# Kernel tuning notes

Measured on AMD Instinct MI355X. Metric: run time of the kernel, lower is better.

## Reference

```python
import jax, jax.numpy as jnp
import numpy as np

EPS = 1e-6
B, T, C = 2, 1024, 2048
H, KV, D = 32, 8, 128
E, F, TOPK = 8, 768, 2


def rmsnorm(x, w):
    xf = x.astype(jnp.float32)
    var = jnp.mean(xf * xf, axis=-1, keepdims=True)
    return w * (xf * jax.lax.rsqrt(var + EPS)).astype(x.dtype)


def rotate_half(x):
    d = x.shape[-1] // 2
    return jnp.concatenate([-x[..., d:], x[..., :d]], axis=-1)


def setup_inputs() -> dict:
    key = jax.random.key(0)
    ks = jax.random.split(key, 12)
    sc = 0.02
    x = jax.random.normal(ks[0], (B, T, C), dtype=jnp.float32)
    # RoPE tables: cos/sin of shape [B, T, D]
    inv_freq = 1.0 / (1e6 ** (np.arange(0, D, 2, dtype=np.float32) / D))
    pos = np.arange(T, dtype=np.float32)
    freqs = pos[:, None] * inv_freq[None, :]          # [T, D/2]
    emb = np.concatenate([freqs, freqs], axis=-1)     # [T, D]
    cos = jnp.broadcast_to(jnp.cos(emb)[None], (B, T, D)).astype(jnp.float32)
    sin = jnp.broadcast_to(jnp.sin(emb)[None], (B, T, D)).astype(jnp.float32)
    return {
        "x": x, "cos": cos, "sin": sin,
        "ln1_w": jnp.ones((C,), jnp.float32),
        "q_w": jax.random.normal(ks[1], (C, H * D), jnp.float32) * sc,
        "k_w": jax.random.normal(ks[2], (C, KV * D), jnp.float32) * sc,
        "v_w": jax.random.normal(ks[3], (C, KV * D), jnp.float32) * sc,
        "o_w": jax.random.normal(ks[4], (H * D, C), jnp.float32) * sc,
        "qn_w": jnp.ones((D,), jnp.float32),
        "kn_w": jnp.ones((D,), jnp.float32),
        "ln2_w": jnp.ones((C,), jnp.float32),
        "gate_w": jax.random.normal(ks[5], (C, E), jnp.float32) * sc,
        "gate_up_w": jax.random.normal(ks[6], (E, C, 2 * F), jnp.float32) * sc,
        "down_w": jax.random.normal(ks[7], (E, F, C), jnp.float32) * sc,
    }


def reference(x, cos, sin, ln1_w, q_w, k_w, v_w, o_w, qn_w, kn_w, ln2_w,
              gate_w, gate_up_w, down_w):
    b, t, c = x.shape
    # ---- attention branch ----
    h = rmsnorm(x, ln1_w)
    q = (h @ q_w).reshape(b, t, H, D)
    k = (h @ k_w).reshape(b, t, KV, D)
    v = (h @ v_w).reshape(b, t, KV, D)
    q = rmsnorm(q, qn_w)
    k = rmsnorm(k, kn_w)
    cb = cos[:, :, None, :]
    sb = sin[:, :, None, :]
    q = q * cb + rotate_half(q) * sb
    k = k * cb + rotate_half(k) * sb
    rep = H // KV
    k = jnp.repeat(k, rep, axis=2)  # [b,t,H,D]
    v = jnp.repeat(v, rep, axis=2)
    scores = jnp.einsum('bthd,bshd->bhts', q, k) / jnp.sqrt(jnp.float32(D))
    causal = jnp.tril(jnp.ones((t, t), dtype=bool))
    scores = jnp.where(causal, scores, jnp.finfo(scores.dtype).min)
    attn = jax.nn.softmax(scores, axis=-1)
    ao = jnp.einsum('bhts,bshd->bthd', attn, v).reshape(b, t, H * D) @ o_w
    x = x + ao
    # ---- MoE branch ----
    h2 = rmsnorm(x, ln2_w)
    hidden = h2.reshape(-1, c)                     # [N, C]
    logits = hidden @ gate_w                       # [N, E]
    rw = jax.nn.softmax(logits.astype(jnp.float32), axis=-1)
    tw, ti = jax.lax.top_k(rw, TOPK)
    tw = tw / (tw.sum(axis=-1, keepdims=True) + 1e-9)
    n = hidden.shape[0]
    routed = jnp.zeros_like(logits).at[jnp.arange(n)[:, None], ti].set(tw.astype(logits.dtype))
    routed = routed / (routed.sum(axis=-1, keepdims=True) + 1e-9)
    gu = jnp.einsum('th,ehq->teq', hidden, gate_up_w)   # [N, E, 2F]
    g, u = jnp.split(gu, 2, axis=-1)
    eo = jnp.einsum('teq,eqh->teh', jax.nn.silu(g) * u, down_w)  # [N, E, C]
    moe = (eo * routed[..., None]).sum(axis=1).reshape(b, t, c)
    return x + moe
```

## Files before the change

kernel.cpp:

```cpp
#include <hip/hip_runtime.h>
#include <hip/hip_bf16.h>

typedef short bf16x8 __attribute__((ext_vector_type(8)));
typedef float f32x4 __attribute__((ext_vector_type(4)));
typedef unsigned short u16;

#define NTOK 2048
#define CDIM 2048
#define TSEQ 1024
#define NH   32
#define NKV  8
#define DH   128
#define NE   8
#define FDIM 768
#define CAP  2048

#define GLOAD_LDS16(g, l) \
  __builtin_amdgcn_global_load_lds((const __attribute__((address_space(1))) void*)(g), \
                                   (__attribute__((address_space(3))) void*)(l), 16, 0, 0)

__device__ __forceinline__ u16 f2bf(float f){
  union { float f; unsigned u; } v; v.f = f;
  unsigned r = v.u + 0x7FFFu + ((v.u >> 16) & 1u);
  return (u16)(r >> 16);
}
__device__ __forceinline__ float bf2f(u16 x){
  union { unsigned u; float f; } v; v.u = ((unsigned)x) << 16; return v.f;
}

__device__ __forceinline__ f32x4 mfma_bf16(bf16x8 a, bf16x8 b, f32x4 c){
  return __builtin_amdgcn_mfma_f32_16x16x32_bf16(a, b, c, 0, 0, 0);
}

__device__ __forceinline__ int xcd_swz(int orig, int nwg){
  int xcd = orig & 7;
  int q = nwg >> 3, r = nwg & 7;
  int base = (xcd < r) ? xcd*(q+1) : r*(q+1) + (xcd-r)*q;
  return base + (orig >> 3);
}

__global__ void cast_transpose(const float* __restrict__ in, u16* __restrict__ out,
                               int R, int Cc, int rstride, int d1,
                               long long s_hi, long long s_lo)
{
  __shared__ u16 tile[64][72];
  int z = blockIdx.z;
  in  += (long long)(z / d1) * s_hi + (long long)(z % d1) * s_lo;
  out += (size_t)z * R * Cc;
  int r0 = blockIdx.y*64, c0 = blockIdx.x*64;
  int lr = threadIdx.x >> 4;
  int lc = (threadIdx.x & 15) * 4;
  #pragma unroll
  for(int i=0;i<4;i++){
    int r = lr + i*16;
    float4 v = *(const float4*)(in + (size_t)(r0 + r)*rstride + c0 + lc);
    tile[lc+0][r] = f2bf(v.x);
    tile[lc+1][r] = f2bf(v.y);
    tile[lc+2][r] = f2bf(v.z);
    tile[lc+3][r] = f2bf(v.w);
  }
  __syncthreads();
  int oc  = threadIdx.x >> 2;
  int orr = (threadIdx.x & 3) * 16;
  uint4 a  = *(const uint4*)&tile[oc][orr];
  uint4 b2 = *(const uint4*)&tile[oc][orr + 8];
  *(uint4*)(out + (size_t)(c0+oc)*R + r0 + orr)     = a;
  *(uint4*)(out + (size_t)(c0+oc)*R + r0 + orr + 8) = b2;
}

__global__ void cast_transpose_qkv(const float* __restrict__ qw, const float* __restrict__ kw,
                                   const float* __restrict__ vw, u16* __restrict__ wqkvT)
{
  __shared__ u16 tile[64][72];
  int bx = blockIdx.x;
  const float* in; u16* out; int rstride, c0;
  if(bx < 64){       in = qw; out = wqkvT;                        rstride = 4096; c0 = bx*64; }
  else if(bx < 80){  in = kw; out = wqkvT + (size_t)4096*2048;    rstride = 1024; c0 = (bx-64)*64; }
  else {             in = vw; out = wqkvT + (size_t)5120*2048;    rstride = 1024; c0 = (bx-80)*64; }
  const int R = 2048;
  int r0 = blockIdx.y*64;
  int lr = threadIdx.x >> 4;
  int lc = (threadIdx.x & 15) * 4;
  #pragma unroll
  for(int i=0;i<4;i++){
    int r = lr + i*16;
    float4 v = *(const float4*)(in + (size_t)(r0 + r)*rstride + c0 + lc);
    tile[lc+0][r] = f2bf(v.x);
    tile[lc+1][r] = f2bf(v.y);
    tile[lc+2][r] = f2bf(v.z);
    tile[lc+3][r] = f2bf(v.w);
  }
  __syncthreads();
  int oc  = threadIdx.x >> 2;
  int orr = (threadIdx.x & 3) * 16;
  uint4 a  = *(const uint4*)&tile[oc][orr];
  uint4 b2 = *(const uint4*)&tile[oc][orr + 8];
  *(uint4*)(out + (size_t)(c0+oc)*R + r0 + orr)     = a;
  *(uint4*)(out + (size_t)(c0+oc)*R + r0 + orr + 8) = b2;
}

__global__ void transpose_gate(const float* __restrict__ gw, float* __restrict__ gwT)
{
  int i = blockIdx.x*256 + threadIdx.x;
  int c = i >> 3, e = i & 7;
  gwT[(size_t)e*CDIM + c] = gw[(size_t)c*NE + e];
}

__global__ void transpose_u16(const u16* __restrict__ in, u16* __restrict__ out,
                              int R, int Cc, int rstride, int d1,
                              long long s_hi, long long s_lo)
{
  __shared__ u16 tile[32][34];
  int z = blockIdx.z;
  in += (long long)(z / d1) * s_hi + (long long)(z % d1) * s_lo;
  out += (size_t)z * R * Cc;
  int tx = threadIdx.x & 31, ty = threadIdx.x >> 5;
  int r0 = blockIdx.y * 32, c0 = blockIdx.x * 32;
  #pragma unroll
  for(int i=0;i<4;i++){
    int r = r0 + ty + i*8;
    if(r < R && c0 + tx < Cc) tile[ty + i*8][tx] = in[(size_t)r * rstride + c0 + tx];
  }
  __syncthreads();
  #pragma unroll
  for(int i=0;i<4;i++){
    int c = c0 + ty + i*8;
    if(c < Cc && r0 + tx < R) out[(size_t)c * R + r0 + tx] = tile[tx][ty + i*8];
  }
}

__global__ void rmsnorm_kernel(const float* __restrict__ x, const float* __restrict__ w,
                               u16* __restrict__ outb, float* __restrict__ outf)
{
  __shared__ float sbuf[4];
  int row = blockIdx.x;
  const float* xr = x + (size_t)row * CDIM;
  int t0 = threadIdx.x * 8;
  float4 v0 = *(const float4*)(xr + t0);
  float4 v1 = *(const float4*)(xr + t0 + 4);
  float a[8] = {v0.x,v0.y,v0.z,v0.w,v1.x,v1.y,v1.z,v1.w};
  float ss = 0.f;
  #pragma unroll
  for(int i=0;i<8;i++) ss += a[i]*a[i];
  #pragma unroll
  for(int o=32;o>0;o>>=1) ss += __shfl_xor(ss, o);
  if((threadIdx.x & 63) == 0) sbuf[threadIdx.x >> 6] = ss;
  __syncthreads();
  float tot = sbuf[0]+sbuf[1]+sbuf[2]+sbuf[3];
  float r = rsqrtf(tot * (1.0f/CDIM) + 1e-6f);
  float4 w0 = *(const float4*)(w + t0);
  float4 w1 = *(const float4*)(w + t0 + 4);
  float wv[8] = {w0.x,w0.y,w0.z,w0.w,w1.x,w1.y,w1.z,w1.w};
  #pragma unroll
  for(int i=0;i<8;i++){
    float o = a[i] * r * wv[i];
    outb[(size_t)row*CDIM + t0 + i] = f2bf(o);
    if(outf) outf[(size_t)row*CDIM + t0 + i] = o;
  }
}

__global__ __launch_bounds__(512, 1) void gemm256(const u16* __restrict__ A,
                                                  const u16* __restrict__ Bt,
                                                  u16* __restrict__ Cb,
                                                  int M, int N, int K)
{
  extern __shared__ u16 lds[];
  const int NT = K >> 6;
  int tid = threadIdx.x;
  int lane = tid & 63, g = lane >> 4, cl = lane & 15;
  int wid = tid >> 6, wr = wid >> 2, wc = wid & 3;
  int br = blockIdx.y * 256, bc = blockIdx.x * 192;
  int rowl[4], slotl[4], srcoff[4];
  #pragma unroll
  for(int l=0;l<4;l++){
    int c = l*512 + tid;
    rowl[l]  = c >> 3;
    slotl[l] = c & 7;
    srcoff[l] = (slotl[l] ^ (rowl[l] & 7)) * 8;
  }
  f32x4 acc[8][3];
  #pragma unroll
  for(int m=0;m<8;m++)
    #pragma unroll
    for(int n=0;n<3;n++) acc[m][n] = (f32x4){0.f,0.f,0.f,0.f};

  auto stage = [&](int t, int b){
    int k0 = t << 6;
    #pragma unroll
    for(int l=0;l<4;l++)
      GLOAD_LDS16(A  + (size_t)(br + rowl[l])*K + k0 + srcoff[l],
                  &lds[b*16384 + rowl[l]*64 + slotl[l]*8]);
    #pragma unroll
    for(int l=0;l<3;l++)
      GLOAD_LDS16(Bt + (size_t)(bc + rowl[l])*K + k0 + srcoff[l],
                  &lds[32768 + b*12288 + rowl[l]*64 + slotl[l]*8]);
  };

  stage(0, 0);
  for(int t=0;t<NT;t++){
    int buf = t & 1;
    if(t+1 < NT){
      stage(t+1, buf^1);
      asm volatile("s_waitcnt vmcnt(7)" ::: "memory");
    } else {
      asm volatile("s_waitcnt vmcnt(0)" ::: "memory");
    }
    asm volatile("s_barrier" ::: "memory");
    const u16* As_ = &lds[buf*16384];
    const u16* Bs_ = &lds[32768 + buf*12288];
    __builtin_amdgcn_s_setprio(1);
    #pragma unroll
    for(int kk=0;kk<2;kk++){
      bf16x8 a[8], b[3];
      #pragma unroll
      for(int m=0;m<8;m++){
        int row = wr*128 + m*16 + cl;
        int sl  = ((4*kk + g) ^ (row & 7)) * 8;
        a[m] = *(const bf16x8*)&As_[row*64 + sl];
      }
      #pragma unroll
      for(int n=0;n<3;n++){
        int row = wc*48 + n*16 + cl;
        int sl  = ((4*kk + g) ^ (row & 7)) * 8;
        b[n] = *(const bf16x8*)&Bs_[row*64 + sl];
      }
      #pragma unroll
      for(int m=0;m<8;m++)
        #pragma unroll
        for(int n=0;n<3;n++)
          acc[m][n] = mfma_bf16(a[m], b[n], acc[m][n]);
    }
    __builtin_amdgcn_s_setprio(0);
    asm volatile("s_barrier" ::: "memory");
  }
  #pragma unroll
  for(int m=0;m<8;m++)
    #pragma unroll
    for(int n=0;n<3;n++)
      #pragma unroll
      for(int j=0;j<4;j++){
        int row = br + wr*128 + m*16 + g*4 + j;
        int col = bc + wc*48 + n*16 + cl;
        Cb[(size_t)row*N + col] = f2bf(acc[m][n][j]);
      }
}

__global__ __launch_bounds__(256) void gemm_oproj_pipe(const u16* __restrict__ A,
                                                       const u16* __restrict__ Bt,
                                                       float* __restrict__ C,
                                                       const float* __restrict__ addsrc,
                                                       int M, int N, int K)
{
  extern __shared__ u16 lds[];
  int nwg = gridDim.x;
  int wgid = xcd_swz(blockIdx.x, nwg);
  int nbx = N >> 7;
  int bys = wgid / nbx, bxs = wgid % nbx;
  const int NT = K >> 6;
  int tid = threadIdx.x;
  int lane = tid&63, g = lane>>4, cl = lane&15;
  int w = tid>>6, wr = w>>1, wc = w&1;
  int br = bys*128, bc = bxs*128;
  int rowc[4], slotc[4], srcoff[4];
  #pragma unroll
  for(int l=0;l<4;l++){
    int c = l*256 + tid;
    rowc[l]  = c >> 3;
    slotc[l] = c & 7;
    srcoff[l] = (slotc[l] ^ (rowc[l] & 7)) * 8;
  }
  f32x4 acc[4][4];
  #pragma unroll
  for(int m=0;m<4;m++)
    #pragma unroll
    for(int n=0;n<4;n++) acc[m][n] = (f32x4){0.f,0.f,0.f,0.f};

  auto stage = [&](int t, int b){
    int k0 = t << 6;
    #pragma unroll
    for(int l=0;l<4;l++)
      GLOAD_LDS16(A + (size_t)(br + rowc[l])*K + k0 + srcoff[l],
                  &lds[b*8192 + rowc[l]*64 + slotc[l]*8]);
    #pragma unroll
    for(int l=0;l<4;l++)
      GLOAD_LDS16(Bt + (size_t)(bc + rowc[l])*K + k0 + srcoff[l],
                  &lds[16384 + b*8192 + rowc[l]*64 + slotc[l]*8]);
  };

  stage(0, 0);
  for(int t=0;t<NT;t++){
    int buf = t & 1;
    if(t+1 < NT){
      stage(t+1, buf^1);
      asm volatile("s_waitcnt vmcnt(8)" ::: "memory");
    } else {
      asm volatile("s_waitcnt vmcnt(0)" ::: "memory");
    }
    asm volatile("s_barrier" ::: "memory");
    const u16* As_ = &lds[buf*8192];
    const u16* Bs_ = &lds[16384 + buf*8192];
    __builtin_amdgcn_s_setprio(1);
    #pragma unroll
    for(int kk=0;kk<2;kk++){
      bf16x8 a[4], b[4];
      #pragma unroll
      for(int m=0;m<4;m++){
        int row = wr*64 + m*16 + cl;
        int sl  = ((4*kk + g) ^ (row & 7)) * 8;
        a[m] = *(const bf16x8*)&As_[row*64 + sl];
      }
      #pragma unroll
      for(int n=0;n<4;n++){
        int row = wc*64 + n*16 + cl;
        int sl  = ((4*kk + g) ^ (row & 7)) * 8;
        b[n] = *(const bf16x8*)&Bs_[row*64 + sl];
      }
      #pragma unroll
      for(int m=0;m<4;m++)
        #pragma unroll
        for(int n=0;n<4;n++)
          acc[m][n] = mfma_bf16(a[m], b[n], acc[m][n]);
    }
    __builtin_amdgcn_s_setprio(0);
    asm volatile("s_barrier" ::: "memory");
  }
  #pragma unroll
  for(int m=0;m<4;m++)
    #pragma unroll
    for(int n=0;n<4;n++)
      #pragma unroll
      for(int j=0;j<4;j++){
        int row = br + wr*64 + m*16 + g*4 + j;
        int col = bc + wc*64 + n*16 + cl;
        C[(size_t)row*N + col] = acc[m][n][j] + addsrc[(size_t)row*N + col];
      }
}

__global__ void qk_norm_rope(const u16* __restrict__ qkv, const float* __restrict__ cosb,
                             const float* __restrict__ sinb, const float* __restrict__ qnw,
                             const float* __restrict__ knw,
                             u16* __restrict__ qb, u16* __restrict__ kb)
{
  __shared__ float red[2];
  __shared__ float buf[128];
  int bt = blockIdx.x;
  int head = blockIdx.y;
  int d = threadIdx.x;
  int b = bt >> 10, t = bt & 1023;
  bool isq = head < NH;
  const u16* src = qkv + (size_t)bt*6144 + (isq ? head*DH : 4096 + (head-NH)*DH);
  float v = bf2f(src[d]);
  float ss = v*v;
  #pragma unroll
  for(int o=32;o>0;o>>=1) ss += __shfl_xor(ss, o);
  if((threadIdx.x & 63) == 0) red[threadIdx.x >> 6] = ss;
  __syncthreads();
  float tot = red[0] + red[1];
  float r = rsqrtf(tot * (1.0f/DH) + 1e-6f);
  float nv = v * r * (isq ? qnw[d] : knw[d]);
  buf[d] = nv;
  __syncthreads();
  float rot = (d < 64) ? -buf[d+64] : buf[d-64];
  float cs = cosb[(size_t)bt*DH + d], sn = sinb[(size_t)bt*DH + d];
  float ov = nv*cs + rot*sn;
  if(isq) ov *= 0.08838834764831845f;
  if(isq) qb[(((size_t)b*NH  + head)     *TSEQ + t)*DH + d] = f2bf(ov);
  else    kb[(((size_t)b*NKV + (head-NH))*TSEQ + t)*DH + d] = f2bf(ov);
}

__global__ __launch_bounds__(256) void attn_kernel(const u16* __restrict__ qb,
                                                   const u16* __restrict__ kb,
                                                   const u16* __restrict__ vt,
                                                   u16* __restrict__ aob)
{
  __shared__ u16 Ks[64*128];
  __shared__ u16 Vs[144*64];
  __shared__ u16 Ps[4][32][72];
  int tid = threadIdx.x;
  int w = tid>>6, lane = tid&63, g = lane>>4, cl = lane&15;
  int nwg = gridDim.x * gridDim.y * gridDim.z;
  int orig = (blockIdx.z * gridDim.y + blockIdx.y) * gridDim.x + blockIdx.x;
  int wgid = xcd_swz(orig, nwg);
  int bxs = wgid % gridDim.x;
  int bys = (wgid / gridDim.x) % gridDim.y;
  int bzs = wgid / (gridDim.x * gridDim.y);
  int b = bzs, kvh = bys;
  int qt = (gridDim.x - 1) - bxs;
  int q0 = qt*32;
  int h = kvh*4 + w;
  const u16* qp = qb + (((size_t)b*NH  + h  )*TSEQ)*DH;
  const u16* kp = kb + (((size_t)b*NKV + kvh)*TSEQ)*DH;
  const u16* vp = vt + (((size_t)b*NKV + kvh)*DH)*TSEQ;
  for(int idx = tid; idx < 16*64; idx += 256){
    int r = idx >> 6, c2 = idx & 63;
    Vs[(128 + r)*64 + c2] = (r == 0) ? (u16)0x3F80 : (u16)0;
  }
  int kRow[4], kDst[4], kSrc[4], vRow[4], vDst[4], vSrc[4];
  #pragma unroll
  for(int it=0; it<4; it++){
    int c = tid + it*256;
    kRow[it] = c >> 4;
    int ks = c & 15;
    kDst[it] = kRow[it]*128 + ks*8;
    kSrc[it] = (ks ^ (kRow[it] & 7)) * 8;
    vRow[it] = c >> 3;
    int vs = c & 7;
    vDst[it] = vRow[it]*64 + vs*8;
    vSrc[it] = (vs ^ (vRow[it] & 7)) * 8;
  }
  bf16x8 aq[2][4];
  #pragma unroll
  for(int m=0;m<2;m++)
    #pragma unroll
    for(int kd=0;kd<4;kd++)
      aq[m][kd] = *(const bf16x8*)(qp + (size_t)(q0 + m*16 + cl)*DH + kd*32 + g*8);
  f32x4 accO[2][9];
  #pragma unroll
  for(int m=0;m<2;m++)
    #pragma unroll
    for(int n=0;n<9;n++) accO[m][n] = (f32x4){0.f,0.f,0.f,0.f};
  float mr[2][4];
  #pragma unroll
  for(int m=0;m<2;m++)
    #pragma unroll
    for(int j=0;j<4;j++) mr[m][j] = -1e30f;
  for(int kv0 = 0; kv0 < q0 + 32; kv0 += 64){
    #pragma unroll
    for(int it=0; it<4; it++){
      GLOAD_LDS16(kp + (size_t)(kv0 + kRow[it])*DH + kSrc[it], &Ks[kDst[it]]);
      GLOAD_LDS16(vp + (size_t)vRow[it]*TSEQ + kv0 + vSrc[it], &Vs[vDst[it]]);
    }
    __syncthreads();
    f32x4 sc[2][4];
    #pragma unroll
    for(int m=0;m<2;m++)
      #pragma unroll
      for(int n=0;n<4;n++) sc[m][n] = (f32x4){0.f,0.f,0.f,0.f};
    __builtin_amdgcn_s_setprio(1);
    #pragma unroll
    for(int kd=0;kd<4;kd++){
      bf16x8 bk[4];
      #pragma unroll
      for(int n=0;n<4;n++){
        int row = n*16 + cl;
        bk[n] = *(const bf16x8*)&Ks[row*128 + (((kd*4 + g) ^ (cl & 7))*8)];
      }
      #pragma unroll
      for(int m=0;m<2;m++)
        #pragma unroll
        for(int n=0;n<4;n++)
          sc[m][n] = mfma_bf16(aq[m][kd], bk[n], sc[m][n]);
    }
    __builtin_amdgcn_s_setprio(0);
    if(kv0 + 63 > q0){
      #pragma unroll
      for(int m=0;m<2;m++)
        #pragma unroll
        for(int n=0;n<4;n++)
          #pragma unroll
          for(int j=0;j<4;j++){
            int row = q0 + m*16 + g*4 + j;
            int col = kv0 + n*16 + cl;
            if(col > row) sc[m][n][j] = -1e30f;
          }
    }
    float tmax[2][4];
    #pragma unroll
    for(int m=0;m<2;m++)
      #pragma unroll
      for(int j=0;j<4;j++)
        tmax[m][j] = fmaxf(fmaxf(sc[m][0][j], sc[m][1][j]), fmaxf(sc[m][2][j], sc[m][3][j]));
    #pragma unroll
    for(int o=1;o<16;o<<=1)
      #pragma unroll
      for(int m=0;m<2;m++)
        #pragma unroll
        for(int j=0;j<4;j++) tmax[m][j] = fmaxf(tmax[m][j], __shfl_xor(tmax[m][j], o));
    float grow = -1e30f;
    #pragma unroll
    for(int m=0;m<2;m++)
      #pragma unroll
      for(int j=0;j<4;j++) grow = fmaxf(grow, tmax[m][j] - mr[m][j]);
    grow = fmaxf(grow, __shfl_xor(grow, 16));
    grow = fmaxf(grow, __shfl_xor(grow, 32));
    if(grow > 8.0f){
      #pragma unroll
      for(int m=0;m<2;m++)
        #pragma unroll
        for(int j=0;j<4;j++){
          float mn = fmaxf(mr[m][j], tmax[m][j]);
          float f  = __expf(mr[m][j] - mn);
          mr[m][j] = mn;
          #pragma unroll
          for(int n=0;n<9;n++) accO[m][n][j] *= f;
        }
    }
    #pragma unroll
    for(int m=0;m<2;m++)
      #pragma unroll
      for(int n=0;n<4;n++)
        #pragma unroll
        for(int j=0;j<4;j++)
          sc[m][n][j] = __expf(sc[m][n][j] - mr[m][j]);
    #pragma unroll
    for(int m=0;m<2;m++)
      #pragma unroll
      for(int n=0;n<4;n++)
        #pragma unroll
        for(int j=0;j<4;j++)
          Ps[w][m*16 + g*4 + j][n*16 + cl] = f2bf(sc[m][n][j]);
    bf16x8 pa[2][2];
    #pragma unroll
    for(int m=0;m<2;m++)
      #pragma unroll
      for(int s2=0;s2<2;s2++)
        pa[m][s2] = *(const bf16x8*)&Ps[w][m*16 + cl][s2*32 + g*8];
    __builtin_amdgcn_s_setprio(1);
    #pragma unroll
    for(int n=0;n<9;n++){
      #pragma unroll
      for(int s2=0;s2<2;s2++){
        bf16x8 bv = *(const bf16x8*)&Vs[(n*16 + cl)*64 + (((s2*4 + g) ^ (cl & 7))*8)];
        #pragma unroll
        for(int m=0;m<2;m++)
          accO[m][n] = mfma_bf16(pa[m][s2], bv, accO[m][n]);
      }
    }
    __builtin_amdgcn_s_setprio(0);
    __syncthreads();
  }
  #pragma unroll
  for(int m=0;m<2;m++){
    float linv[4];
    #pragma unroll
    for(int j=0;j<4;j++){
      float l = __shfl(accO[m][8][j], lane & 48);
      linv[j] = 1.0f / l;
    }
    #pragma unroll
    for(int n=0;n<8;n++)
      #pragma unroll
      for(int j=0;j<4;j++){
        int row = q0 + m*16 + g*4 + j;
        float v = accO[m][n][j] * linv[j];
        aob[((size_t)b*TSEQ + row)*(NH*DH) + h*DH + n*16 + cl] = f2bf(v);
      }
  }
}

__global__ void route_kernel(const float* __restrict__ h2f, const float* __restrict__ gwT,
                             int* __restrict__ cnt, int* __restrict__ bidx,
                             float* __restrict__ bw)
{
  int lane = threadIdx.x & 63;
  int token = blockIdx.x*4 + (threadIdx.x >> 6);
  float acc[8];
  #pragma unroll
  for(int e=0;e<8;e++) acc[e]=0.f;
  for(int c0 = lane*4; c0 < CDIM; c0 += 256){
    float4 hv = *(const float4*)(h2f + (size_t)token*CDIM + c0);
    #pragma unroll
    for(int e=0;e<8;e++){
      float4 gv = *(const float4*)(gwT + (size_t)e*CDIM + c0);
      acc[e] += hv.x*gv.x + hv.y*gv.y + hv.z*gv.z + hv.w*gv.w;
    }
  }
  #pragma unroll
  for(int o=32;o>0;o>>=1)
    #pragma unroll
    for(int e=0;e<8;e++) acc[e] += __shfl_xor(acc[e], o);
  if(lane==0){
    float mx = acc[0];
    #pragma unroll
    for(int e=1;e<8;e++) mx = fmaxf(mx, acc[e]);
    float rw[8]; float s=0.f;
    #pragma unroll
    for(int e=0;e<8;e++){ rw[e] = __expf(acc[e]-mx); s += rw[e]; }
    #pragma unroll
    for(int e=0;e<8;e++) rw[e] /= s;
    int i0=0;
    #pragma unroll
    for(int e=1;e<8;e++) if(rw[e] > rw[i0]) i0=e;
    int i1 = (i0==0)?1:0;
    #pragma unroll
    for(int e=0;e<8;e++) if(e!=i0 && rw[e] > rw[i1]) i1=e;
    float tw0=rw[i0], tw1=rw[i1];
    float s1 = tw0+tw1+1e-9f;
    float a0 = tw0/s1, a1 = tw1/s1;
    float s2 = a0+a1+1e-9f;
    float w0 = a0/s2, w1 = a1/s2;
    int sl0 = atomicAdd(&cnt[i0],1);
    bidx[i0*CAP + sl0] = token; bw[i0*CAP + sl0] = w0;
    int sl1 = atomicAdd(&cnt[i1],1);
    bidx[i1*CAP + sl1] = token; bw[i1*CAP + sl1] = w1;
  }
}

__global__ __launch_bounds__(256) void gemm_gateup_pipe(const u16* __restrict__ h2b,
                                                        const u16* __restrict__ gupT,
                                                        u16* __restrict__ act,
                                                        const int* __restrict__ bidx,
                                                        const int* __restrict__ cnt)
{
  extern __shared__ u16 lds[];
  int d = blockIdx.x;
  int e = d & 7, j = d >> 3;
  int y = j / 12, x = j % 12;
  int nc = cnt[e];
  int sr = y*128;
  if(sr >= nc) return;
  const int K = CDIM, NT = K >> 6;
  const u16* Btg = gupT + (size_t)e*1536*CDIM + (size_t)(x*64)*CDIM;
  const u16* Btu = Btg + (size_t)768*CDIM;
  const int* be = bidx + e*CAP;
  int tid = threadIdx.x;
  int lane = tid&63, g = lane>>4, cl = lane&15;
  int w = tid>>6, wr = w>>1, wc = w&1;
  int rowA[4], slotA[4], srcA[4];
  long long atok[4];
  #pragma unroll
  for(int l=0;l<4;l++){
    int c = l*256 + tid;
    rowA[l]  = c >> 3;
    slotA[l] = c & 7;
    srcA[l] = (slotA[l] ^ (rowA[l] & 7)) * 8;
    int t = be[sr + rowA[l]];
    if(t < 0 || t >= NTOK) t = 0;
    atok[l] = (long long)t * CDIM;
  }
  int rowB[2], slotB[2], srcB[2];
  #pragma unroll
  for(int l=0;l<2;l++){
    int c = l*256 + tid;
    rowB[l]  = c >> 3;
    slotB[l] = c & 7;
    srcB[l] = (slotB[l] ^ (rowB[l] & 7)) * 8;
  }
  f32x4 accG[4][2], accU[4][2];
  #pragma unroll
  for(int m=0;m<4;m++)
    #pragma unroll
    for(int n=0;n<2;n++){ accG[m][n] = (f32x4){0.f,0.f,0.f,0.f}; accU[m][n] = (f32x4){0.f,0.f,0.f,0.f}; }

  auto stage = [&](int t, int b){
    int k0 = t << 6;
    #pragma unroll
    for(int l=0;l<4;l++)
      GLOAD_LDS16(h2b + atok[l] + k0 + srcA[l],
                  &lds[b*8192 + rowA[l]*64 + slotA[l]*8]);
    #pragma unroll
    for(int l=0;l<2;l++)
      GLOAD_LDS16(Btg + (size_t)rowB[l]*K + k0 + srcB[l],
                  &lds[16384 + b*4096 + rowB[l]*64 + slotB[l]*8]);
    #pragma unroll
    for(int l=0;l<2;l++)
      GLOAD_LDS16(Btu + (size_t)rowB[l]*K + k0 + srcB[l],
                  &lds[24576 + b*4096 + rowB[l]*64 + slotB[l]*8]);
  };

  stage(0, 0);
  for(int t=0;t<NT;t++){
    int buf = t & 1;
    if(t+1 < NT){
      stage(t+1, buf^1);
      asm volatile("s_waitcnt vmcnt(8)" ::: "memory");
    } else {
      asm volatile("s_waitcnt vmcnt(0)" ::: "memory");
    }
    asm volatile("s_barrier" ::: "memory");
    const u16* As_ = &lds[buf*8192];
    const u16* Bg_ = &lds[16384 + buf*4096];
    const u16* Bu_ = &lds[24576 + buf*4096];
    __builtin_amdgcn_s_setprio(1);
    #pragma unroll
    for(int kk=0;kk<2;kk++){
      bf16x8 a[4], bg[2], bu[2];
      #pragma unroll
      for(int m=0;m<4;m++){
        int row = wr*64 + m*16 + cl;
        int sl  = ((4*kk + g) ^ (row & 7)) * 8;
        a[m] = *(const bf16x8*)&As_[row*64 + sl];
      }
      #pragma unroll
      for(int n=0;n<2;n++){
        int row = wc*32 + n*16 + cl;
        int sl  = ((4*kk + g) ^ (row & 7)) * 8;
        bg[n] = *(const bf16x8*)&Bg_[row*64 + sl];
        bu[n] = *(const bf16x8*)&Bu_[row*64 + sl];
      }
      #pragma unroll
      for(int m=0;m<4;m++)
        #pragma unroll
        for(int n=0;n<2;n++){
          accG[m][n] = mfma_bf16(a[m], bg[n], accG[m][n]);
          accU[m][n] = mfma_bf16(a[m], bu[n], accU[m][n]);
        }
    }
    __builtin_amdgcn_s_setprio(0);
    asm volatile("s_barrier" ::: "memory");
  }
  #pragma unroll
  for(int m=0;m<4;m++)
    #pragma unroll
    for(int n=0;n<2;n++)
      #pragma unroll
      for(int jj=0;jj<4;jj++){
        int slot = sr + wr*64 + m*16 + g*4 + jj;
        int col  = x*64 + wc*32 + n*16 + cl;
        float gv = accG[m][n][jj], uv = accU[m][n][jj];
        float av = gv / (1.f + __expf(-gv)) * uv;
        act[((size_t)e*CAP + slot)*FDIM + col] = f2bf(av);
      }
}

__global__ __launch_bounds__(256) void gemm_down_pipe(const u16* __restrict__ act,
                                                      const u16* __restrict__ downT,
                                                      float* __restrict__ out,
                                                      const int* __restrict__ bidx,
                                                      const float* __restrict__ bw,
                                                      const int* __restrict__ cnt)
{
  extern __shared__ u16 lds[];
  int d = blockIdx.x;
  int e = d & 7, j = d >> 3;
  int y = j >> 4, x = j & 15;
  int nc = cnt[e];
  int sr = y*128;
  if(sr >= nc) return;
  const int K = FDIM, NT = K >> 6;
  const u16* A  = act   + ((size_t)e*CAP + sr)*FDIM;
  const u16* Bt = downT + (size_t)e*CDIM*FDIM + (size_t)(x*128)*FDIM;
  const int* be = bidx + e*CAP;
  const float* bwe = bw + e*CAP;
  int tid = threadIdx.x;
  int lane = tid&63, g = lane>>4, cl = lane&15;
  int w = tid>>6, wr = w>>1, wc = w&1;
  int rowc[4], slotc[4], srcoff[4];
  #pragma unroll
  for(int l=0;l<4;l++){
    int c = l*256 + tid;
    rowc[l]  = c >> 3;
    slotc[l] = c & 7;
    srcoff[l] = (slotc[l] ^ (rowc[l] & 7)) * 8;
  }
  f32x4 acc[4][4];
  #pragma unroll
  for(int m=0;m<4;m++)
    #pragma unroll
    for(int n=0;n<4;n++) acc[m][n] = (f32x4){0.f,0.f,0.f,0.f};

  auto stage = [&](int t, int b){
    int k0 = t << 6;
    #pragma unroll
    for(int l=0;l<4;l++)
      GLOAD_LDS16(A + (size_t)rowc[l]*K + k0 + srcoff[l],
                  &lds[b*8192 + rowc[l]*64 + slotc[l]*8]);
    #pragma unroll
    for(int l=0;l<4;l++)
      GLOAD_LDS16(Bt + (size_t)rowc[l]*K + k0 + srcoff[l],
                  &lds[16384 + b*8192 + rowc[l]*64 + slotc[l]*8]);
  };

  stage(0, 0);
  for(int t=0;t<NT;t++){
    int buf = t & 1;
    if(t+1 < NT){
      stage(t+1, buf^1);
      asm volatile("s_waitcnt vmcnt(8)" ::: "memory");
    } else {
      asm volatile("s_waitcnt vmcnt(0)" ::: "memory");
    }
    asm volatile("s_barrier" ::: "memory");
    const u16* As_ = &lds[buf*8192];
    const u16* Bs_ = &lds[16384 + buf*8192];
    __builtin_amdgcn_s_setprio(1);
    #pragma unroll
    for(int kk=0;kk<2;kk++){
      bf16x8 a[4], b[4];
      #pragma unroll
      for(int m=0;m<4;m++){
        int row = wr*64 + m*16 + cl;
        int sl  = ((4*kk + g) ^ (row & 7)) * 8;
        a[m] = *(const bf16x8*)&As_[row*64 + sl];
      }
      #pragma unroll
      for(int n=0;n<4;n++){
        int row = wc*64 + n*16 + cl;
        int sl  = ((4*kk + g) ^ (row & 7)) * 8;
        b[n] = *(const bf16x8*)&Bs_[row*64 + sl];
      }
      #pragma unroll
      for(int m=0;m<4;m++)
        #pragma unroll
        for(int n=0;n<4;n++)
          acc[m][n] = mfma_bf16(a[m], b[n], acc[m][n]);
    }
    __builtin_amdgcn_s_setprio(0);
    asm volatile("s_barrier" ::: "memory");
  }
  #pragma unroll
  for(int m=0;m<4;m++)
    #pragma unroll
    for(int jj=0;jj<4;jj++){
      int slot = sr + wr*64 + m*16 + g*4 + jj;
      if(slot < nc){
        int tok = be[slot];
        float wgt = bwe[slot];
        #pragma unroll
        for(int n=0;n<4;n++){
          int col = x*128 + wc*64 + n*16 + cl;
          atomicAdd(out + (size_t)tok*CDIM + col, wgt * acc[m][n][jj]);
        }
      }
    }
}

extern "C" void kernel_launch(void* const* d_in, const int* in_sizes, int n_in,
                              void* d_out, int out_size, void* d_ws, size_t ws_size,
                              hipStream_t stream)
{
  const float* x     = (const float*)d_in[0];
  const float* cosb  = (const float*)d_in[1];
  const float* sinb  = (const float*)d_in[2];
  const float* ln1w  = (const float*)d_in[3];
  const float* qw    = (const float*)d_in[4];
  const float* kw    = (const float*)d_in[5];
  const float* vw    = (const float*)d_in[6];
  const float* ow    = (const float*)d_in[7];
  const float* qnw   = (const float*)d_in[8];
  const float* knw   = (const float*)d_in[9];
  const float* ln2w  = (const float*)d_in[10];
  const float* gatew = (const float*)d_in[11];
  const float* gupw  = (const float*)d_in[12];
  const float* downw = (const float*)d_in[13];
  float* out = (float*)d_out;

  char* ws = (char*)d_ws;
  size_t off = 0;
  auto alloc = [&](size_t bytes)->char*{
    char* p = ws + off;
    off = (off + bytes + 255) & ~(size_t)255;
    return p;
  };
  u16*   wqkvT = (u16*)  alloc((size_t)6144*2048*2);
  u16*   owT   = (u16*)  alloc((size_t)2048*4096*2);
  u16*   gupT  = (u16*)  alloc((size_t)8*1536*2048*2);
  u16*   downT = (u16*)  alloc((size_t)8*2048*768*2);
  u16*   h1b   = (u16*)  alloc((size_t)2048*2048*2);
  u16*   qkvb  = (u16*)  alloc((size_t)2048*6144*2);
  u16*   qb    = (u16*)  alloc((size_t)2*32*1024*128*2);
  u16*   kb    = (u16*)  alloc((size_t)2*8*1024*128*2);
  u16*   vt    = (u16*)  alloc((size_t)2*8*1024*128*2);
  u16*   aob   = (u16*)  alloc((size_t)2048*4096*2);
  float* h2f   = (float*)alloc((size_t)2048*2048*4);
  u16*   h2b   = (u16*)  alloc((size_t)2048*2048*2);
  u16*   actb  = (u16*)  alloc((size_t)8*2048*768*2);
  int*   bidx  = (int*)  alloc((size_t)8*2048*4);
  float* bwgt  = (float*)alloc((size_t)8*2048*4);
  float* gwT   = (float*)alloc((size_t)8*2048*4);
  int*   cnt   = (int*)  alloc(64);
  (void)ws_size; (void)in_sizes; (void)n_in; (void)out_size;

  hipMemsetAsync(cnt, 0, 8*sizeof(int), stream);

  cast_transpose_qkv<<<dim3(96,32), 256, 0, stream>>>(qw, kw, vw, wqkvT);
  cast_transpose<<<dim3(32,64,1), 256, 0, stream>>>(ow, owT,      4096, 2048, 2048, 1, 0, 0);
  cast_transpose<<<dim3(24,32,8), 256, 0, stream>>>(gupw, gupT,   2048, 1536, 1536, 8, 0, (long long)2048*1536);
  cast_transpose<<<dim3(32,12,8), 256, 0, stream>>>(downw, downT, 768,  2048, 2048, 8, 0, (long long)768*2048);
  transpose_gate<<<64, 256, 0, stream>>>(gatew, gwT);

  rmsnorm_kernel<<<2048, 256, 0, stream>>>(x, ln1w, h1b, nullptr);
  gemm256<<<dim3(32,8), 512, 114688, stream>>>(h1b, wqkvT, qkvb, 2048, 6144, 2048);
  qk_norm_rope<<<dim3(2048,40), 128, 0, stream>>>(qkvb, cosb, sinb, qnw, knw, qb, kb);
  transpose_u16<<<dim3(4,32,16), 256, 0, stream>>>(qkvb + 5120, vt, 1024, 128, 6144, 8,
                                                   (long long)1024*6144, 128);
  attn_kernel<<<dim3(32,8,2), 256, 0, stream>>>(qb, kb, vt, aob);
  gemm_oproj_pipe<<<256, 256, 65536, stream>>>(aob, owT, out, x, 2048, 2048, 4096);
  rmsnorm_kernel<<<2048, 256, 0, stream>>>(out, ln2w, h2b, h2f);
  route_kernel<<<512, 256, 0, stream>>>(h2f, gwT, cnt, bidx, bwgt);
  gemm_gateup_pipe<<<1536, 256, 65536, stream>>>(h2b, gupT, actb, bidx, cnt);
  gemm_down_pipe<<<2048, 256, 65536, stream>>>(actb, downT, out, bidx, bwgt, cnt);
}
```

Baseline: 442.3 us.

## Replace 256x192 QKV GEMM with 128x128 tiles and XCD-swizzled 1D grid

The QKV projection GEMM moves from a 256x192 tile run by 512 threads (256 workgroups, one per CU) to a 128x128 tile run by 256 threads on a 1D grid of 768 workgroups, with an XCD-aware block swizzle. The smaller tile and smaller LDS footprint allow more workgroups per CU and better L2 locality across XCDs, which is meant to improve occupancy and load balance. In exchange, per-tile arithmetic intensity falls, so global and LDS traffic per MFMA rises.

```diff
diff --git a/kernel.cpp b/kernel.cpp
--- a/kernel.cpp
+++ b/kernel.cpp
@@ -159,41 +159,45 @@
   }
 }
 
-__global__ __launch_bounds__(512, 1) void gemm256(const u16* __restrict__ A,
-                                                  const u16* __restrict__ Bt,
-                                                  u16* __restrict__ Cb,
-                                                  int M, int N, int K)
+__global__ __launch_bounds__(256) void gemm_qkv_pipe(const u16* __restrict__ A,
+                                                     const u16* __restrict__ Bt,
+                                                     u16* __restrict__ Cb,
+                                                     int M, int N, int K)
 {
   extern __shared__ u16 lds[];
+  int nwg = gridDim.x;
+  int wgid = xcd_swz(blockIdx.x, nwg);
+  int nbx = N >> 7;
+  int bys = wgid / nbx, bxs = wgid % nbx;
   const int NT = K >> 6;
   int tid = threadIdx.x;
-  int lane = tid & 63, g = lane >> 4, cl = lane & 15;
-  int wid = tid >> 6, wr = wid >> 2, wc = wid & 3;
-  int br = blockIdx.y * 256, bc = blockIdx.x * 192;
-  int rowl[4], slotl[4], srcoff[4];
+  int lane = tid&63, g = lane>>4, cl = lane&15;
+  int w = tid>>6, wr = w>>1, wc = w&1;
+  int br = bys*128, bc = bxs*128;
+  int rowc[4], slotc[4], srcoff[4];
   #pragma unroll
   for(int l=0;l<4;l++){
-    int c = l*512 + tid;
-    rowl[l]  = c >> 3;
-    slotl[l] = c & 7;
-    srcoff[l] = (slotl[l] ^ (rowl[l] & 7)) * 8;
-  }
-  f32x4 acc[8][3];
-  #pragma unroll
-  for(int m=0;m<8;m++)
-    #pragma unroll
-    for(int n=0;n<3;n++) acc[m][n] = (f32x4){0.f,0.f,0.f,0.f};
+    int c = l*256 + tid;
+    rowc[l]  = c >> 3;
+    slotc[l] = c & 7;
+    srcoff[l] = (slotc[l] ^ (rowc[l] & 7)) * 8;
+  }
+  f32x4 acc[4][4];
+  #pragma unroll
+  for(int m=0;m<4;m++)
+    #pragma unroll
+    for(int n=0;n<4;n++) acc[m][n] = (f32x4){0.f,0.f,0.f,0.f};
 
   auto stage = [&](int t, int b){
     int k0 = t << 6;
     #pragma unroll
     for(int l=0;l<4;l++)
-      GLOAD_LDS16(A  + (size_t)(br + rowl[l])*K + k0 + srcoff[l],
-                  &lds[b*16384 + rowl[l]*64 + slotl[l]*8]);
-    #pragma unroll
-    for(int l=0;l<3;l++)
-      GLOAD_LDS16(Bt + (size_t)(bc + rowl[l])*K + k0 + srcoff[l],
-                  &lds[32768 + b*12288 + rowl[l]*64 + slotl[l]*8]);
+      GLOAD_LDS16(A + (size_t)(br + rowc[l])*K + k0 + srcoff[l],
+                  &lds[b*8192 + rowc[l]*64 + slotc[l]*8]);
+    #pragma unroll
+    for(int l=0;l<4;l++)
+      GLOAD_LDS16(Bt + (size_t)(bc + rowc[l])*K + k0 + srcoff[l],
+                  &lds[16384 + b*8192 + rowc[l]*64 + slotc[l]*8]);
   };
 
   stage(0, 0);
@@ -201,46 +205,46 @@
     int buf = t & 1;
     if(t+1 < NT){
       stage(t+1, buf^1);
-      asm volatile("s_waitcnt vmcnt(7)" ::: "memory");
+      asm volatile("s_waitcnt vmcnt(8)" ::: "memory");
     } else {
       asm volatile("s_waitcnt vmcnt(0)" ::: "memory");
     }
     asm volatile("s_barrier" ::: "memory");
-    const u16* As_ = &lds[buf*16384];
-    const u16* Bs_ = &lds[32768 + buf*12288];
+    const u16* As_ = &lds[buf*8192];
+    const u16* Bs_ = &lds[16384 + buf*8192];
     __builtin_amdgcn_s_setprio(1);
     #pragma unroll
     for(int kk=0;kk<2;kk++){
-      bf16x8 a[8], b[3];
-      #pragma unroll
-      for(int m=0;m<8;m++){
-        int row = wr*128 + m*16 + cl;
+      bf16x8 a[4], b[4];
+      #pragma unroll
+      for(int m=0;m<4;m++){
+        int row = wr*64 + m*16 + cl;
         int sl  = ((4*kk + g) ^ (row & 7)) * 8;
         a[m] = *(const bf16x8*)&As_[row*64 + sl];
       }
       #pragma unroll
-      for(int n=0;n<3;n++){
-        int row = wc*48 + n*16 + cl;
+      for(int n=0;n<4;n++){
+        int row = wc*64 + n*16 + cl;
         int sl  = ((4*kk + g) ^ (row & 7)) * 8;
         b[n] = *(const bf16x8*)&Bs_[row*64 + sl];
       }
       #pragma unroll
-      for(int m=0;m<8;m++)
-        #pragma unroll
-        for(int n=0;n<3;n++)
+      for(int m=0;m<4;m++)
+        #pragma unroll
+        for(int n=0;n<4;n++)
           acc[m][n] = mfma_bf16(a[m], b[n], acc[m][n]);
     }
     __builtin_amdgcn_s_setprio(0);
     asm volatile("s_barrier" ::: "memory");
   }
   #pragma unroll
-  for(int m=0;m<8;m++)
-    #pragma unroll
-    for(int n=0;n<3;n++)
+  for(int m=0;m<4;m++)
+    #pragma unroll
+    for(int n=0;n<4;n++)
       #pragma unroll
       for(int j=0;j<4;j++){
-        int row = br + wr*128 + m*16 + g*4 + j;
-        int col = bc + wc*48 + n*16 + cl;
+        int row = br + wr*64 + m*16 + g*4 + j;
+        int col = bc + wc*64 + n*16 + cl;
         Cb[(size_t)row*N + col] = f2bf(acc[m][n][j]);
       }
 }
@@ -870,7 +874,7 @@
   transpose_gate<<<64, 256, 0, stream>>>(gatew, gwT);
 
   rmsnorm_kernel<<<2048, 256, 0, stream>>>(x, ln1w, h1b, nullptr);
-  gemm256<<<dim3(32,8), 512, 114688, stream>>>(h1b, wqkvT, qkvb, 2048, 6144, 2048);
+  gemm_qkv_pipe<<<768, 256, 65536, stream>>>(h1b, wqkvT, qkvb, 2048, 6144, 2048);
   qk_norm_rope<<<dim3(2048,40), 128, 0, stream>>>(qkvb, cosb, sinb, qnw, knw, qb, kb);
   transpose_u16<<<dim3(4,32,16), 256, 0, stream>>>(qkvb + 5120, vt, 1024, 128, 6144, 8,
                                                    (long long)1024*6144, 128);
```

Measured after the change: 451.9 us. 2.2% more time.

## Double-buffer K/V tiles and balance causal work by pairing query tiles

Applied to the files above, without the earlier changes.

The attention kernel now uses 512-thread workgroups where each wave handles 16 query rows of one head. Each workgroup processes two query tiles (pr and 31-pr) so causal work is balanced across blocks. K/V tiles are double-buffered in dynamic LDS, with the next tile's global-to-LDS loads issued before computing the current one and explicit vmcnt waits and barriers. This aims to hide load latency and remove tail imbalance, at the cost of more LDS per block and fewer MFMAs reusing each K/V fragment per wave.

```diff
diff --git a/kernel.cpp b/kernel.cpp
--- a/kernel.cpp
+++ b/kernel.cpp
@@ -368,14 +368,12 @@
   else    kb[(((size_t)b*NKV + (head-NH))*TSEQ + t)*DH + d] = f2bf(ov);
 }
 
-__global__ __launch_bounds__(256) void attn_kernel(const u16* __restrict__ qb,
+__global__ __launch_bounds__(512) void attn_kernel(const u16* __restrict__ qb,
                                                    const u16* __restrict__ kb,
                                                    const u16* __restrict__ vt,
                                                    u16* __restrict__ aob)
 {
-  __shared__ u16 Ks[64*128];
-  __shared__ u16 Vs[144*64];
-  __shared__ u16 Ps[4][32][72];
+  extern __shared__ u16 lds[];
   int tid = threadIdx.x;
   int w = tid>>6, lane = tid&63, g = lane>>4, cl = lane&15;
   int nwg = gridDim.x * gridDim.y * gridDim.z;
@@ -384,21 +382,22 @@
   int bxs = wgid % gridDim.x;
   int bys = (wgid / gridDim.x) % gridDim.y;
   int bzs = wgid / (gridDim.x * gridDim.y);
-  int b = bzs, kvh = bys;
-  int qt = (gridDim.x - 1) - bxs;
-  int q0 = qt*32;
-  int h = kvh*4 + w;
-  const u16* qp = qb + (((size_t)b*NH  + h  )*TSEQ)*DH;
+  int b = bzs, kvh = bys, pr = bxs;
+  int head = kvh*4 + (w>>1);
+  int mh = w & 1;
+  const u16* qp = qb + (((size_t)b*NH  + head)*TSEQ)*DH;
   const u16* kp = kb + (((size_t)b*NKV + kvh)*TSEQ)*DH;
   const u16* vp = vt + (((size_t)b*NKV + kvh)*DH)*TSEQ;
-  for(int idx = tid; idx < 16*64; idx += 256){
-    int r = idx >> 6, c2 = idx & 63;
-    Vs[(128 + r)*64 + c2] = (r == 0) ? (u16)0x3F80 : (u16)0;
-  }
-  int kRow[4], kDst[4], kSrc[4], vRow[4], vDst[4], vSrc[4];
-  #pragma unroll
-  for(int it=0; it<4; it++){
-    int c = tid + it*256;
+  u16* Psw = &lds[34816 + w*16*72];
+  for(int idx = tid; idx < 2*16*64; idx += 512){
+    int bufi = idx >> 10, rr = (idx >> 6) & 15, c2 = idx & 63;
+    lds[16384 + bufi*9216 + (128 + rr)*64 + c2] = (rr == 0) ? (u16)0x3F80 : (u16)0;
+  }
+  __syncthreads();
+  int kRow[2], kDst[2], kSrc[2], vRow[2], vDst[2], vSrc[2];
+  #pragma unroll
+  for(int it=0; it<2; it++){
+    int c = tid + it*512;
     kRow[it] = c >> 4;
     int ks = c & 15;
     kDst[it] = kRow[it]*128 + ks*8;
@@ -408,142 +407,133 @@
     vDst[it] = vRow[it]*64 + vs*8;
     vSrc[it] = (vs ^ (vRow[it] & 7)) * 8;
   }
-  bf16x8 aq[2][4];
-  #pragma unroll
-  for(int m=0;m<2;m++)
+  int qts[2] = { pr, 31 - pr };
+  for(int ti=0; ti<2; ti++){
+    int qt = qts[ti];
+    int q0 = qt*32;
+    int qr0 = q0 + mh*16;
+    const int NTk = (q0 + 95) >> 6;
+    bf16x8 aq[4];
     #pragma unroll
     for(int kd=0;kd<4;kd++)
-      aq[m][kd] = *(const bf16x8*)(qp + (size_t)(q0 + m*16 + cl)*DH + kd*32 + g*8);
-  f32x4 accO[2][9];
-  #pragma unroll
-  for(int m=0;m<2;m++)
-    #pragma unroll
-    for(int n=0;n<9;n++) accO[m][n] = (f32x4){0.f,0.f,0.f,0.f};
-  float mr[2][4];
-  #pragma unroll
-  for(int m=0;m<2;m++)
-    #pragma unroll
-    for(int j=0;j<4;j++) mr[m][j] = -1e30f;
-  for(int kv0 = 0; kv0 < q0 + 32; kv0 += 64){
-    #pragma unroll
-    for(int it=0; it<4; it++){
-      GLOAD_LDS16(kp + (size_t)(kv0 + kRow[it])*DH + kSrc[it], &Ks[kDst[it]]);
-      GLOAD_LDS16(vp + (size_t)vRow[it]*TSEQ + kv0 + vSrc[it], &Vs[vDst[it]]);
-    }
-    __syncthreads();
-    f32x4 sc[2][4];
-    #pragma unroll
-    for(int m=0;m<2;m++)
-      #pragma unroll
-      for(int n=0;n<4;n++) sc[m][n] = (f32x4){0.f,0.f,0.f,0.f};
-    __builtin_amdgcn_s_setprio(1);
-    #pragma unroll
-    for(int kd=0;kd<4;kd++){
-      bf16x8 bk[4];
-      #pragma unroll
-      for(int n=0;n<4;n++){
-        int row = n*16 + cl;
-        bk[n] = *(const bf16x8*)&Ks[row*128 + (((kd*4 + g) ^ (cl & 7))*8)];
-      }
-      #pragma unroll
-      for(int m=0;m<2;m++)
+      aq[kd] = *(const bf16x8*)(qp + (size_t)(qr0 + cl)*DH + kd*32 + g*8);
+    f32x4 accO[9];
+    #pragma unroll
+    for(int n=0;n<9;n++) accO[n] = (f32x4){0.f,0.f,0.f,0.f};
+    float mr[4];
+    #pragma unroll
+    for(int j=0;j<4;j++) mr[j] = -1e30f;
+    #pragma unroll
+    for(int it=0; it<2; it++){
+      GLOAD_LDS16(kp + (size_t)kRow[it]*DH + kSrc[it], &lds[kDst[it]]);
+      GLOAD_LDS16(vp + (size_t)vRow[it]*TSEQ + vSrc[it], &lds[16384 + vDst[it]]);
+    }
+    for(int t=0; t<NTk; t++){
+      int buf = t & 1;
+      int kv0 = t*64;
+      if(t+1 < NTk){
+        int kv1 = kv0 + 64, nb = buf ^ 1;
+        #pragma unroll
+        for(int it=0; it<2; it++){
+          GLOAD_LDS16(kp + (size_t)(kv1 + kRow[it])*DH + kSrc[it], &lds[nb*8192 + kDst[it]]);
+          GLOAD_LDS16(vp + (size_t)vRow[it]*TSEQ + kv1 + vSrc[it], &lds[16384 + nb*9216 + vDst[it]]);
+        }
+        asm volatile("s_waitcnt vmcnt(4)" ::: "memory");
+      } else {
+        asm volatile("s_waitcnt vmcnt(0)" ::: "memory");
+      }
+      asm volatile("s_barrier" ::: "memory");
+      const u16* Ksb = &lds[buf*8192];
+      const u16* Vsb = &lds[16384 + buf*9216];
+      f32x4 sc[4];
+      #pragma unroll
+      for(int n=0;n<4;n++) sc[n] = (f32x4){0.f,0.f,0.f,0.f};
+      __builtin_amdgcn_s_setprio(1);
+      #pragma unroll
+      for(int kd=0;kd<4;kd++){
+        bf16x8 bk[4];
+        #pragma unroll
+        for(int n=0;n<4;n++){
+          int row = n*16 + cl;
+          bk[n] = *(const bf16x8*)&Ksb[row*128 + (((kd*4 + g) ^ (cl & 7))*8)];
+        }
         #pragma unroll
         for(int n=0;n<4;n++)
-          sc[m][n] = mfma_bf16(aq[m][kd], bk[n], sc[m][n]);
-    }
-    __builtin_amdgcn_s_setprio(0);
-    if(kv0 + 63 > q0){
-      #pragma unroll
-      for(int m=0;m<2;m++)
+          sc[n] = mfma_bf16(aq[kd], bk[n], sc[n]);
+      }
+      __builtin_amdgcn_s_setprio(0);
+      if(kv0 + 63 > q0){
         #pragma unroll
         for(int n=0;n<4;n++)
           #pragma unroll
           for(int j=0;j<4;j++){
-            int row = q0 + m*16 + g*4 + j;
+            int row = qr0 + g*4 + j;
             int col = kv0 + n*16 + cl;
-            if(col > row) sc[m][n][j] = -1e30f;
+            if(col > row) sc[n][j] = -1e30f;
           }
-    }
-    float tmax[2][4];
-    #pragma unroll
-    for(int m=0;m<2;m++)
+      }
+      float tmax[4];
       #pragma unroll
       for(int j=0;j<4;j++)
-        tmax[m][j] = fmaxf(fmaxf(sc[m][0][j], sc[m][1][j]), fmaxf(sc[m][2][j], sc[m][3][j]));
-    #pragma unroll
-    for(int o=1;o<16;o<<=1)
-      #pragma unroll
-      for(int m=0;m<2;m++)
-        #pragma unroll
-        for(int j=0;j<4;j++) tmax[m][j] = fmaxf(tmax[m][j], __shfl_xor(tmax[m][j], o));
-    float grow = -1e30f;
-    #pragma unroll
-    for(int m=0;m<2;m++)
-      #pragma unroll
-      for(int j=0;j<4;j++) grow = fmaxf(grow, tmax[m][j] - mr[m][j]);
-    grow = fmaxf(grow, __shfl_xor(grow, 16));
-    grow = fmaxf(grow, __shfl_xor(grow, 32));
-    if(grow > 8.0f){
-      #pragma unroll
-      for(int m=0;m<2;m++)
+        tmax[j] = fmaxf(fmaxf(sc[0][j], sc[1][j]), fmaxf(sc[2][j], sc[3][j]));
+      #pragma unroll
+      for(int o=1;o<16;o<<=1)
+        #pragma unroll
+        for(int j=0;j<4;j++) tmax[j] = fmaxf(tmax[j], __shfl_xor(tmax[j], o));
+      float grow = -1e30f;
+      #pragma unroll
+      for(int j=0;j<4;j++) grow = fmaxf(grow, tmax[j] - mr[j]);
+      grow = fmaxf(grow, __shfl_xor(grow, 16));
+      grow = fmaxf(grow, __shfl_xor(grow, 32));
+      if(grow > 8.0f){
         #pragma unroll
         for(int j=0;j<4;j++){
-          float mn = fmaxf(mr[m][j], tmax[m][j]);
-          float f  = __expf(mr[m][j] - mn);
-          mr[m][j] = mn;
+          float mn = fmaxf(mr[j], tmax[j]);
+          float f  = __expf(mr[j] - mn);
+          mr[j] = mn;
           #pragma unroll
-          for(int n=0;n<9;n++) accO[m][n][j] *= f;
+          for(int n=0;n<9;n++) accO[n][j] *= f;
         }
-    }
-    #pragma unroll
-    for(int m=0;m<2;m++)
+      }
       #pragma unroll
       for(int n=0;n<4;n++)
         #pragma unroll
         for(int j=0;j<4;j++)
-          sc[m][n][j] = __expf(sc[m][n][j] - mr[m][j]);
-    #pragma unroll
-    for(int m=0;m<2;m++)
+          sc[n][j] = __expf(sc[n][j] - mr[j]);
       #pragma unroll
       for(int n=0;n<4;n++)
         #pragma unroll
         for(int j=0;j<4;j++)
-          Ps[w][m*16 + g*4 + j][n*16 + cl] = f2bf(sc[m][n][j]);
-    bf16x8 pa[2][2];
-    #pragma unroll
-    for(int m=0;m<2;m++)
+          Psw[(g*4 + j)*72 + n*16 + cl] = f2bf(sc[n][j]);
+      bf16x8 pa[2];
       #pragma unroll
       for(int s2=0;s2<2;s2++)
-        pa[m][s2] = *(const bf16x8*)&Ps[w][m*16 + cl][s2*32 + g*8];
-    __builtin_amdgcn_s_setprio(1);
-    #pragma unroll
-    for(int n=0;n<9;n++){
-      #pragma unroll
-      for(int s2=0;s2<2;s2++){
-        bf16x8 bv = *(const bf16x8*)&Vs[(n*16 + cl)*64 + (((s2*4 + g) ^ (cl & 7))*8)];
-        #pragma unroll
-        for(int m=0;m<2;m++)
-          accO[m][n] = mfma_bf16(pa[m][s2], bv, accO[m][n]);
-      }
-    }
-    __builtin_amdgcn_s_setprio(0);
-    __syncthreads();
-  }
-  #pragma unroll
-  for(int m=0;m<2;m++){
+        pa[s2] = *(const bf16x8*)&Psw[cl*72 + s2*32 + g*8];
+      __builtin_amdgcn_s_setprio(1);
+      #pragma unroll
+      for(int n=0;n<9;n++){
+        #pragma unroll
+        for(int s2=0;s2<2;s2++){
+          bf16x8 bv = *(const bf16x8*)&Vsb[(n*16 + cl)*64 + (((s2*4 + g) ^ (cl & 7))*8)];
+          accO[n] = mfma_bf16(pa[s2], bv, accO[n]);
+        }
+      }
+      __builtin_amdgcn_s_setprio(0);
+      asm volatile("s_barrier" ::: "memory");
+    }
     float linv[4];
     #pragma unroll
     for(int j=0;j<4;j++){
-      float l = __shfl(accO[m][8][j], lane & 48);
+      float l = __shfl(accO[8][j], lane & 48);
       linv[j] = 1.0f / l;
     }
     #pragma unroll
     for(int n=0;n<8;n++)
       #pragma unroll
       for(int j=0;j<4;j++){
-        int row = q0 + m*16 + g*4 + j;
-        float v = accO[m][n][j] * linv[j];
-        aob[((size_t)b*TSEQ + row)*(NH*DH) + h*DH + n*16 + cl] = f2bf(v);
+        int row = qr0 + g*4 + j;
+        float v = accO[n][j] * linv[j];
+        aob[((size_t)b*TSEQ + row)*(NH*DH) + head*DH + n*16 + cl] = f2bf(v);
       }
   }
 }
@@ -874,7 +864,7 @@
   qk_norm_rope<<<dim3(2048,40), 128, 0, stream>>>(qkvb, cosb, sinb, qnw, knw, qb, kb);
   transpose_u16<<<dim3(4,32,16), 256, 0, stream>>>(qkvb + 5120, vt, 1024, 128, 6144, 8,
                                                    (long long)1024*6144, 128);
-  attn_kernel<<<dim3(32,8,2), 256, 0, stream>>>(qb, kb, vt, aob);
+  attn_kernel<<<dim3(16,8,2), 512, 88064, stream>>>(qb, kb, vt, aob);
   gemm_oproj_pipe<<<256, 256, 65536, stream>>>(aob, owT, out, x, 2048, 2048, 4096);
   rmsnorm_kernel<<<2048, 256, 0, stream>>>(out, ln2w, h2b, h2f);
   route_kernel<<<512, 256, 0, stream>>>(h2f, gwT, cnt, bidx, bwgt);
```

Result: faster. 432.5 us, median of 3 (-2.2%).
